# Kernel tuning notes

Hardware: AMD Instinct MI355X
Metric: run time of the kernel (lower is better)

Reference implementation:

```python
import jax, jax.numpy as jnp
import numpy as np

MARGIN = 0.2
N = 512
D = 128
N_CLASSES = 64


def setup_inputs() -> dict:
    key = jax.random.key(0)
    k1, k2 = jax.random.split(key)
    z = jax.random.normal(k1, (N, D), dtype=jnp.float32)
    labels = jax.random.randint(k2, (N,), 0, N_CLASSES)
    return {"z": z, "labels": labels}


def _pdist(x, y):
    sq = (jnp.sum(x * x, axis=1)[:, None]
          + jnp.sum(y * y, axis=1)[None, :]
          - 2.0 * (x @ y.T))
    sq = jnp.maximum(sq, 0.0)
    pos = sq > 0
    # safe sqrt (diagonal is exactly 0; avoid inf gradient there)
    return jnp.sqrt(jnp.where(pos, sq, 1.0)) * pos


def reference(z, labels):
    n = labels.shape[0]
    d = _pdist(z, z)                                  # [N, N]
    same = labels[None, :] == labels[:, None]         # [N, N]
    diff = ~same
    same = same & ~jnp.eye(n, dtype=bool)             # fill_diagonal_(False)
    # valid triplet mask [anchor, pos, neg]
    mask = same[:, :, None] & diff[:, None, :]        # [N, N, N] bool
    # d(a,p) - d(a,n) + margin over all (a,p,n)
    losses = d[:, :, None] - d[:, None, :] + MARGIN   # [N, N, N]
    n_eg = jnp.sum((losses > 0) & mask)
    n_triplets = jnp.sum(mask).astype(losses.dtype)
    loss = jnp.sum(jnp.where(mask, jax.nn.relu(losses), 0.0)) / n_triplets
    return loss, n_eg
```

## Files before the change

kernel.cpp:

```cpp
#include <hip/hip_runtime.h>

#define NPTS 512
#define DIM 128
#define MARGIN 0.2f
#define TROWS 64
#define NTILE (NPTS / TROWS)
#define NTHR 512
#define NBLK NPTS

__global__ __launch_bounds__(NTHR, 4) void triplet_partial_kernel(
    const float* __restrict__ z, const int* __restrict__ labels,
    float* __restrict__ psum, unsigned* __restrict__ pcnt,
    unsigned* __restrict__ pntrip)
{
    __shared__ float4 stage[2][TROWS * 32];
    __shared__ float drow[NPTS];
    __shared__ __align__(16) float pdm[NPTS];
    __shared__ int wcnt[8];
    __shared__ float red_f[8];
    __shared__ unsigned red_c[8];

    const int t = threadIdx.x;
    const int a = blockIdx.x;
    const int wid = t >> 6, lane = t & 63;
    const int r = t >> 3;
    const int q = t & 7;
    const int rx = r & 7;

    const float4* zg = reinterpret_cast<const float4*>(z);

    const int lt = labels[t];
    const int la = labels[a];

    float4 za[4];
    #pragma unroll
    for (int kk = 0; kk < 4; ++kk)
        za[kk] = zg[(size_t)a * 32 + q * 4 + kk];

    #pragma unroll
    for (int p = 0; p < 4; ++p) {
        int f = p * NTHR + t;
        int row = f >> 5, ch = f & 31;
        stage[0][row * 32 + (ch ^ (row & 7))] = zg[f];
    }
    __syncthreads();

    for (int T = 0; T < NTILE; ++T) {
        const int cur = T & 1;
        float4 pf[4];
        if (T + 1 < NTILE) {
            #pragma unroll
            for (int p = 0; p < 4; ++p)
                pf[p] = zg[(size_t)(T + 1) * (TROWS * 32) + p * NTHR + t];
        }
        float acc = 0.f;
        #pragma unroll
        for (int kk = 0; kk < 4; ++kk) {
            float4 v = stage[cur][r * 32 + ((q * 4 + kk) ^ rx)];
            float4 w = za[kk];
            float d0 = w.x - v.x, d1 = w.y - v.y, d2 = w.z - v.z, d3 = w.w - v.w;
            acc += d0 * d0 + d1 * d1 + d2 * d2 + d3 * d3;
        }
        acc += __shfl_xor(acc, 1, 64);
        acc += __shfl_xor(acc, 2, 64);
        acc += __shfl_xor(acc, 4, 64);
        if (q == 0) drow[T * TROWS + r] = sqrtf(acc);
        if (T + 1 < NTILE) {
            #pragma unroll
            for (int p = 0; p < 4; ++p) {
                int f = p * NTHR + t;
                int row = f >> 5, ch = f & 31;
                stage[cur ^ 1][row * 32 + (ch ^ (row & 7))] = pf[p];
            }
        }
        __syncthreads();
    }

    const bool pred = (lt == la) && (t != a);
    const unsigned long long m = __ballot(pred);
    if (lane == 0) wcnt[wid] = (int)__popcll(m);
    __syncthreads();

    unsigned base = 0, np = 0;
    #pragma unroll
    for (int w = 0; w < 8; ++w) {
        unsigned cw = (unsigned)wcnt[w];
        if (w < wid) base += cw;
        np += cw;
    }
    const unsigned npad = (np + 3u) & ~3u;
    if (pred)
        pdm[base + __popcll(m & ((1ull << lane) - 1ull))] = drow[t] + MARGIN;
    if ((unsigned)t >= np && (unsigned)t < npad)
        pdm[t] = -1e30f;
    __syncthreads();

    float sum = 0.f;
    unsigned cnt = 0;
    if (lt != la) {
        const float si = drow[t];
        const float4* p4 = reinterpret_cast<const float4*>(pdm);
        const int n4 = (int)(npad >> 2);
        for (int p = 0; p < n4; ++p) {
            float4 qv = p4[p];
            float v0 = qv.x - si, v1 = qv.y - si, v2 = qv.z - si, v3 = qv.w - si;
            if (v0 > 0.f) { sum += v0; ++cnt; }
            if (v1 > 0.f) { sum += v1; ++cnt; }
            if (v2 > 0.f) { sum += v2; ++cnt; }
            if (v3 > 0.f) { sum += v3; ++cnt; }
        }
    }

    #pragma unroll
    for (int off = 32; off > 0; off >>= 1) {
        sum += __shfl_down(sum, off, 64);
        cnt += __shfl_down(cnt, off, 64);
    }
    if (lane == 0) { red_f[wid] = sum; red_c[wid] = cnt; }
    __syncthreads();
    if (t == 0) {
        float S = 0.f;
        unsigned C = 0;
        #pragma unroll
        for (int w = 0; w < 8; ++w) { S += red_f[w]; C += red_c[w]; }
        psum[a] = S;
        pcnt[a] = C;
        pntrip[a] = np * (unsigned)(NPTS - 1 - np);
    }
}

__global__ __launch_bounds__(512) void triplet_final_kernel(
    const float* __restrict__ psum, const unsigned* __restrict__ pcnt,
    const unsigned* __restrict__ pntrip, float* __restrict__ out)
{
    __shared__ float rf[8];
    __shared__ unsigned rc[8], rn[8];

    const int t = threadIdx.x;
    float s = psum[t];
    unsigned c = pcnt[t];
    unsigned nt = pntrip[t];

    #pragma unroll
    for (int off = 32; off > 0; off >>= 1) {
        s  += __shfl_down(s,  off, 64);
        c  += __shfl_down(c,  off, 64);
        nt += __shfl_down(nt, off, 64);
    }
    const int wid = t >> 6, lane = t & 63;
    if (lane == 0) { rf[wid] = s; rc[wid] = c; rn[wid] = nt; }
    __syncthreads();
    if (t == 0) {
        double S = 0.0;
        unsigned C = 0, NT = 0;
        #pragma unroll
        for (int w = 0; w < 8; ++w) { S += (double)rf[w]; C += rc[w]; NT += rn[w]; }
        out[0] = (float)(S / (double)NT);
        out[1] = (float)C;
    }
}

extern "C" void kernel_launch(void* const* d_in, const int* in_sizes, int n_in,
                              void* d_out, int out_size, void* d_ws, size_t ws_size,
                              hipStream_t stream) {
    const float* z = (const float*)d_in[0];
    const int* labels = (const int*)d_in[1];
    float* out = (float*)d_out;

    float* psum = (float*)d_ws;
    unsigned* pcnt = (unsigned*)((char*)d_ws + NBLK * sizeof(float));
    unsigned* pntrip = pcnt + NBLK;

    triplet_partial_kernel<<<NBLK, NTHR, 0, stream>>>(z, labels, psum, pcnt, pntrip);
    triplet_final_kernel<<<1, NPTS, 0, stream>>>(psum, pcnt, pntrip, out);
}
```

Measured before the change: 16.83 us.

## Pre-transpose embeddings so each thread computes one full distance directly

Adds a small transpose kernel that writes z in a [D/4][N] float4 layout to workspace. The main kernel then has each thread stream its own point's 32 float4 values with coalesced loads and compute its distance to the anchor alone. This removes the double-buffered LDS tile loop, the per-tile barriers and the shuffle reductions. In exchange it adds an extra kernel launch and a global round trip of z, and every block now reads the whole transposed matrix from cache.

```diff
diff --git a/kernel.cpp b/kernel.cpp
--- a/kernel.cpp
+++ b/kernel.cpp
@@ -3,18 +3,38 @@
 #define NPTS 512
 #define DIM 128
 #define MARGIN 0.2f
-#define TROWS 64
-#define NTILE (NPTS / TROWS)
 #define NTHR 512
-#define NBLK NPTS
+
+__global__ __launch_bounds__(512) void transpose_kernel(
+    const float* __restrict__ z, float4* __restrict__ zt4)
+{
+    __shared__ float4 lds[64 * 33];
+    const int t = threadIdx.x;
+    const int b = blockIdx.x;
+    const float4* z4 = reinterpret_cast<const float4*>(z);
+
+    #pragma unroll
+    for (int i = 0; i < 4; ++i) {
+        int f = i * 512 + t;
+        int row = f >> 5, kk = f & 31;
+        lds[row * 33 + kk] = z4[b * 2048 + f];
+    }
+    __syncthreads();
+    #pragma unroll
+    for (int i = 0; i < 4; ++i) {
+        int w = i * 512 + t;
+        int kk = w >> 6, c = w & 63;
+        zt4[kk * NPTS + b * 64 + c] = lds[c * 33 + kk];
+    }
+}
 
 __global__ __launch_bounds__(NTHR, 4) void triplet_partial_kernel(
-    const float* __restrict__ z, const int* __restrict__ labels,
+    const float4* __restrict__ zt4, const float* __restrict__ z,
+    const int* __restrict__ labels,
     float* __restrict__ psum, unsigned* __restrict__ pcnt,
     unsigned* __restrict__ pntrip)
 {
-    __shared__ float4 stage[2][TROWS * 32];
-    __shared__ float drow[NPTS];
+    __shared__ float4 za4[DIM / 4];
     __shared__ __align__(16) float pdm[NPTS];
     __shared__ int wcnt[8];
     __shared__ float red_f[8];
@@ -23,58 +43,24 @@
     const int t = threadIdx.x;
     const int a = blockIdx.x;
     const int wid = t >> 6, lane = t & 63;
-    const int r = t >> 3;
-    const int q = t & 7;
-    const int rx = r & 7;
-
-    const float4* zg = reinterpret_cast<const float4*>(z);
 
     const int lt = labels[t];
     const int la = labels[a];
 
-    float4 za[4];
-    #pragma unroll
-    for (int kk = 0; kk < 4; ++kk)
-        za[kk] = zg[(size_t)a * 32 + q * 4 + kk];
-
-    #pragma unroll
-    for (int p = 0; p < 4; ++p) {
-        int f = p * NTHR + t;
-        int row = f >> 5, ch = f & 31;
-        stage[0][row * 32 + (ch ^ (row & 7))] = zg[f];
-    }
+    if (t < DIM / 4)
+        za4[t] = reinterpret_cast<const float4*>(z)[(size_t)a * (DIM / 4) + t];
     __syncthreads();
 
-    for (int T = 0; T < NTILE; ++T) {
-        const int cur = T & 1;
-        float4 pf[4];
-        if (T + 1 < NTILE) {
-            #pragma unroll
-            for (int p = 0; p < 4; ++p)
-                pf[p] = zg[(size_t)(T + 1) * (TROWS * 32) + p * NTHR + t];
-        }
-        float acc = 0.f;
-        #pragma unroll
-        for (int kk = 0; kk < 4; ++kk) {
-            float4 v = stage[cur][r * 32 + ((q * 4 + kk) ^ rx)];
-            float4 w = za[kk];
-            float d0 = w.x - v.x, d1 = w.y - v.y, d2 = w.z - v.z, d3 = w.w - v.w;
-            acc += d0 * d0 + d1 * d1 + d2 * d2 + d3 * d3;
-        }
-        acc += __shfl_xor(acc, 1, 64);
-        acc += __shfl_xor(acc, 2, 64);
-        acc += __shfl_xor(acc, 4, 64);
-        if (q == 0) drow[T * TROWS + r] = sqrtf(acc);
-        if (T + 1 < NTILE) {
-            #pragma unroll
-            for (int p = 0; p < 4; ++p) {
-                int f = p * NTHR + t;
-                int row = f >> 5, ch = f & 31;
-                stage[cur ^ 1][row * 32 + (ch ^ (row & 7))] = pf[p];
-            }
-        }
-        __syncthreads();
+    float4 acc4 = make_float4(0.f, 0.f, 0.f, 0.f);
+    #pragma unroll
+    for (int kk = 0; kk < DIM / 4; ++kk) {
+        float4 v = zt4[kk * NPTS + t];
+        float4 w = za4[kk];
+        float d0 = w.x - v.x, d1 = w.y - v.y, d2 = w.z - v.z, d3 = w.w - v.w;
+        acc4.x += d0 * d0; acc4.y += d1 * d1;
+        acc4.z += d2 * d2; acc4.w += d3 * d3;
     }
+    const float d = sqrtf((acc4.x + acc4.y) + (acc4.z + acc4.w));
 
     const bool pred = (lt == la) && (t != a);
     const unsigned long long m = __ballot(pred);
@@ -90,7 +76,7 @@
     }
     const unsigned npad = (np + 3u) & ~3u;
     if (pred)
-        pdm[base + __popcll(m & ((1ull << lane) - 1ull))] = drow[t] + MARGIN;
+        pdm[base + __popcll(m & ((1ull << lane) - 1ull))] = d + MARGIN;
     if ((unsigned)t >= np && (unsigned)t < npad)
         pdm[t] = -1e30f;
     __syncthreads();
@@ -98,7 +84,7 @@
     float sum = 0.f;
     unsigned cnt = 0;
     if (lt != la) {
-        const float si = drow[t];
+        const float si = d;
         const float4* p4 = reinterpret_cast<const float4*>(pdm);
         const int n4 = (int)(npad >> 2);
         for (int p = 0; p < n4; ++p) {
@@ -167,10 +153,13 @@
     const int* labels = (const int*)d_in[1];
     float* out = (float*)d_out;
 
-    float* psum = (float*)d_ws;
-    unsigned* pcnt = (unsigned*)((char*)d_ws + NBLK * sizeof(float));
-    unsigned* pntrip = pcnt + NBLK;
+    float4* zt4 = (float4*)d_ws;
+    float* psum = (float*)((char*)d_ws + 256 * 1024);
+    unsigned* pcnt = (unsigned*)((char*)d_ws + 256 * 1024 + NPTS * 4);
+    unsigned* pntrip = (unsigned*)((char*)d_ws + 256 * 1024 + NPTS * 8);
 
-    triplet_partial_kernel<<<NBLK, NTHR, 0, stream>>>(z, labels, psum, pcnt, pntrip);
+    transpose_kernel<<<8, 512, 0, stream>>>(z, zt4);
+    triplet_partial_kernel<<<NPTS, NTHR, 0, stream>>>(zt4, z, labels,
+                                                      psum, pcnt, pntrip);
     triplet_final_kernel<<<1, NPTS, 0, stream>>>(psum, pcnt, pntrip, out);
 }
```

Result: slower. 61.25 us (+263.8%).
